# Kernel tuning notes

Hardware: AMD Instinct MI355X
Metric: run time of the kernel (lower is better)

Reference implementation:

```python
import jax, jax.numpy as jnp
import numpy as np

EMBED_DIM = 1024
NUM_HEADS = 16
HEAD_DIM = EMBED_DIM // NUM_HEADS
B, S = 2, 2048


def setup_inputs() -> dict:
    key = jax.random.key(0)
    ks = jax.random.split(key, 9)
    scale = 1.0 / np.sqrt(EMBED_DIM)
    return {
        "x": jax.random.normal(ks[0], (B, S, EMBED_DIM), dtype=jnp.float32),
        "Wq": jax.random.normal(ks[1], (EMBED_DIM, EMBED_DIM), dtype=jnp.float32) * scale,
        "bq": jnp.zeros((EMBED_DIM,), dtype=jnp.float32),
        "Wk": jax.random.normal(ks[2], (EMBED_DIM, EMBED_DIM), dtype=jnp.float32) * scale,
        "bk": jnp.zeros((EMBED_DIM,), dtype=jnp.float32),
        "Wv": jax.random.normal(ks[3], (EMBED_DIM, EMBED_DIM), dtype=jnp.float32) * scale,
        "bv": jnp.zeros((EMBED_DIM,), dtype=jnp.float32),
        "Wo": jax.random.normal(ks[4], (EMBED_DIM, EMBED_DIM), dtype=jnp.float32) * scale,
        "bo": jnp.zeros((EMBED_DIM,), dtype=jnp.float32),
    }


def _split_heads(t):
    # [B, S, E] -> [B, H, S, Dh]
    b, s, _ = t.shape
    return t.reshape(b, s, NUM_HEADS, HEAD_DIM).transpose(0, 2, 1, 3)


def reference(x, Wq, bq, Wk, bk, Wv, bv, Wo, bo):
    q = _split_heads(x @ Wq + bq)
    k = _split_heads(x @ Wk + bk)
    v = _split_heads(x @ Wv + bv)
    scale = jnp.sqrt(jnp.asarray(HEAD_DIM, dtype=x.dtype))
    scores = jnp.einsum("bhqd,bhkd->bhqk", q, k) / scale
    attn = jax.nn.softmax(scores, axis=-1)
    out = jnp.einsum("bhqk,bhkd->bhqd", attn, v)  # [B,H,S,Dh]
    out = out.transpose(0, 2, 1, 3).reshape(x.shape[0], x.shape[1], EMBED_DIM)
    return out @ Wo + bo
```

## Files before the change

### kernel.cpp

```cpp
#include <hip/hip_runtime.h>
#include <math.h>
#include <stdint.h>

typedef __bf16 bf16;
typedef __bf16 bf16x2 __attribute__((ext_vector_type(2)));
typedef __bf16 bf16x4 __attribute__((ext_vector_type(4)));
typedef __bf16 bf16x8 __attribute__((ext_vector_type(8)));
typedef float f32x4 __attribute__((ext_vector_type(4)));
typedef float f32x16 __attribute__((ext_vector_type(16)));

constexpr int E = 1024;
constexpr int S = 2048;
constexpr int H = 16;


__device__ __forceinline__ void gload16(const void* g, void* l) {
  __builtin_amdgcn_global_load_lds(
      (__attribute__((address_space(1))) void*)(uintptr_t)g,
      (__attribute__((address_space(3))) void*)(uint32_t)(uintptr_t)l, 16, 0, 0);
}

__device__ __forceinline__ f32x4 mfma16(bf16x8 a, bf16x8 b, f32x4 c) {
  return __builtin_amdgcn_mfma_f32_16x16x32_bf16(a, b, c, 0, 0, 0);
}
__device__ __forceinline__ f32x16 mfma32(bf16x8 a, bf16x8 b, f32x16 c) {
  return __builtin_amdgcn_mfma_f32_32x32x16_bf16(a, b, c, 0, 0, 0);
}

__device__ __forceinline__ float fexp2(float x) {
#if __has_builtin(__builtin_amdgcn_exp2f)
  return __builtin_amdgcn_exp2f(x);
#else
  float r;
  asm("v_exp_f32 %0, %1" : "=v"(r) : "v"(x));
  return r;
#endif
}

__device__ __forceinline__ uint32_t pkbf(float lo, float hi) {
  bf16x2 p;
  p[0] = (bf16)lo;
  p[1] = (bf16)hi;
  return __builtin_bit_cast(uint32_t, p);
}

__global__ __launch_bounds__(256) void cast_x(const float* __restrict__ x,
                                              bf16* __restrict__ o) {
  const size_t i = ((size_t)blockIdx.x * 256 + threadIdx.x) * 8;
  const float4 a = *(const float4*)(x + i);
  const float4 b = *(const float4*)(x + i + 4);
  bf16x8 r;
  r[0] = (bf16)a.x; r[1] = (bf16)a.y; r[2] = (bf16)a.z; r[3] = (bf16)a.w;
  r[4] = (bf16)b.x; r[5] = (bf16)b.y; r[6] = (bf16)b.z; r[7] = (bf16)b.w;
  *(bf16x8*)(o + i) = r;
}

__global__ __launch_bounds__(256) void transpose_cast_w(
    const float* __restrict__ W0, const float* __restrict__ W1,
    const float* __restrict__ W2, const float* __restrict__ W3,
    bf16* __restrict__ T0, bf16* __restrict__ T1, bf16* __restrict__ T2,
    bf16* __restrict__ T3) {
  const float* W;
  bf16* T;
  switch (blockIdx.z) {
    case 0: W = W0; T = T0; break;
    case 1: W = W1; T = T1; break;
    case 2: W = W2; T = T2; break;
    default: W = W3; T = T3; break;
  }
  __shared__ float t[64][65];
  const int k0 = blockIdx.y * 64, n0 = blockIdx.x * 64;
  const int tr = threadIdx.x >> 4;
  const int tc = (threadIdx.x & 15) * 4;
#pragma unroll
  for (int u = 0; u < 4; ++u) {
    const float4 v = *(const float4*)(W + (size_t)(k0 + tr + u * 16) * E + n0 + tc);
    t[tr + u * 16][tc + 0] = v.x;
    t[tr + u * 16][tc + 1] = v.y;
    t[tr + u * 16][tc + 2] = v.z;
    t[tr + u * 16][tc + 3] = v.w;
  }
  __syncthreads();
#pragma unroll
  for (int u = 0; u < 4; ++u) {
    const int n = tr + u * 16;
    bf16x4 o;
#pragma unroll
    for (int i = 0; i < 4; ++i) o[i] = (bf16)t[tc + i][n];
    *(bf16x4*)(T + (size_t)(n0 + n) * E + k0 + tc) = o;
  }
}

__global__ __launch_bounds__(256) void gemm_qkv(const bf16* __restrict__ A,
                                                const bf16* __restrict__ Wt,
                                                const float* __restrict__ bq,
                                                const float* __restrict__ bk,
                                                const float* __restrict__ bv,
                                                bf16* __restrict__ qo,
                                                bf16* __restrict__ ko,
                                                bf16* __restrict__ vo) {
  __shared__ __attribute__((aligned(16))) bf16 Asm[128 * 32];
  __shared__ __attribute__((aligned(16))) bf16 Bsm[128 * 32];
  const int z = blockIdx.z;
  const bf16* Bt = Wt + (size_t)z * E * E;
  const float* bias = (z == 0) ? bq : (z == 1) ? bk : bv;
  const int tid = threadIdx.x;
  const int w = tid >> 6, lane = tid & 63, quad = lane >> 4, ln = lane & 15;
  const int bm = blockIdx.y * 128, bn = blockIdx.x * 128;
  const int wr = w >> 1, wc = w & 1;
  const int srow = w * 32 + (lane >> 2);
  const int scol = (lane & 3) * 8;
  const bf16* Ag = A + (size_t)(bm + srow) * E + scol;
  const bf16* Bg = Bt + (size_t)(bn + srow) * E + scol;
  f32x4 acc[4][4] = {};

  for (int k0 = 0; k0 < E; k0 += 32) {
    gload16(Ag + k0, &Asm[(w * 32) * 32]);
    gload16(Ag + k0 + (size_t)16 * E, &Asm[(w * 32 + 16) * 32]);
    gload16(Bg + k0, &Bsm[(w * 32) * 32]);
    gload16(Bg + k0 + (size_t)16 * E, &Bsm[(w * 32 + 16) * 32]);
    __syncthreads();
    bf16x8 af[4], bfr[4];
#pragma unroll
    for (int t = 0; t < 4; ++t) {
      af[t] = *(const bf16x8*)&Asm[(wr * 64 + t * 16 + ln) * 32 + quad * 8];
      bfr[t] = *(const bf16x8*)&Bsm[(wc * 64 + t * 16 + ln) * 32 + quad * 8];
    }
#pragma unroll
    for (int rt = 0; rt < 4; ++rt)
#pragma unroll
      for (int ct = 0; ct < 4; ++ct)
        acc[rt][ct] = mfma16(af[rt], bfr[ct], acc[rt][ct]);
    __syncthreads();
  }

  const float scl = (z == 0) ? 0.18033688f : 1.0f;
  const int hglob = (bn + wc * 64) >> 6;
  float bvv[4];
#pragma unroll
  for (int ct = 0; ct < 4; ++ct) bvv[ct] = bias[bn + wc * 64 + ct * 16 + ln];

#pragma unroll
  for (int rt = 0; rt < 4; ++rt) {
    const int row0 = bm + wr * 64 + rt * 16 + quad * 4;
    const int bb = row0 >> 11;
    const int rl = row0 & 2047;
    const size_t hb = (size_t)(bb * 16 + hglob) * 131072;
#pragma unroll
    for (int ct = 0; ct < 4; ++ct) {
      if (z == 2) {
        const int mt = ct >> 1, ln32 = ((ct & 1) << 4) | ln;
        const int tau = rl >> 6, hfv = (rl >> 3) & 1, j0 = rl & 7;
        bf16x4 p;
#pragma unroll
        for (int r = 0; r < 4; ++r) p[r] = (bf16)(acc[rt][ct][r] + bvv[ct]);
        *(bf16x4*)&vo[hb + (size_t)((tau * 8 + mt * 4 + rt) * 512 +
                                    hfv * 256 + ln32 * 8 + j0)] = p;
      } else {
        bf16* o = (z == 0) ? qo : ko;
        const int t = rl >> 5, ln0 = rl & 31;
        const size_t base =
            hb + (size_t)((t * 4 + ct) * 512 + (ln >> 3) * 256 + (ln & 7));
#pragma unroll
        for (int r = 0; r < 4; ++r)
          o[base + (ln0 + r) * 8] = (bf16)((acc[rt][ct][r] + bvv[ct]) * scl);
      }
    }
  }
}

__global__ __launch_bounds__(256) void gemm_wo(const bf16* __restrict__ A,
                                               const bf16* __restrict__ Bt,
                                               const float* __restrict__ bias,
                                               float* __restrict__ C) {
  __shared__ __attribute__((aligned(16))) bf16 Asm[64 * 32];
  __shared__ __attribute__((aligned(16))) bf16 Bsm[128 * 32];
  const int tid = threadIdx.x;
  const int w = tid >> 6, lane = tid & 63, quad = lane >> 4, ln = lane & 15;
  const int bm = blockIdx.y * 64, bn = blockIdx.x * 128;
  const int wr = w >> 1, wc = w & 1;
  const int sr = lane >> 2, sc = (lane & 3) * 8;
  const bf16* Ag = A + (size_t)(bm + w * 16 + sr) * E + sc;
  const bf16* Bg = Bt + (size_t)(bn + w * 32 + sr) * E + sc;
  f32x4 acc[2][4] = {};

  for (int k0 = 0; k0 < E; k0 += 32) {
    gload16(Ag + k0, &Asm[(w * 16) * 32]);
    gload16(Bg + k0, &Bsm[(w * 32) * 32]);
    gload16(Bg + k0 + (size_t)16 * E, &Bsm[(w * 32 + 16) * 32]);
    __syncthreads();
    bf16x8 af[2], bfr[4];
#pragma unroll
    for (int t = 0; t < 2; ++t)
      af[t] = *(const bf16x8*)&Asm[(wr * 32 + t * 16 + ln) * 32 + quad * 8];
#pragma unroll
    for (int t = 0; t < 4; ++t)
      bfr[t] = *(const bf16x8*)&Bsm[(wc * 64 + t * 16 + ln) * 32 + quad * 8];
#pragma unroll
    for (int rt = 0; rt < 2; ++rt)
#pragma unroll
      for (int ct = 0; ct < 4; ++ct)
        acc[rt][ct] = mfma16(af[rt], bfr[ct], acc[rt][ct]);
    __syncthreads();
  }

  float bvv[4];
#pragma unroll
  for (int ct = 0; ct < 4; ++ct) bvv[ct] = bias[bn + wc * 64 + ct * 16 + ln];
#pragma unroll
  for (int rt = 0; rt < 2; ++rt) {
    const int row0 = bm + wr * 32 + rt * 16 + quad * 4;
#pragma unroll
    for (int ct = 0; ct < 4; ++ct) {
      const int c = bn + wc * 64 + ct * 16 + ln;
#pragma unroll
      for (int r = 0; r < 4; ++r)
        C[(size_t)(row0 + r) * E + c] = acc[rt][ct][r] + bvv[ct];
    }
  }
}

__global__ __launch_bounds__(512, 4) void attn_mfma(const bf16* __restrict__ Qf,
                                                    const bf16* __restrict__ Kf,
                                                    const bf16* __restrict__ Vf,
                                                    bf16* __restrict__ Og) {
  __shared__ __attribute__((aligned(16))) char smem[33792];

  const int tid = threadIdx.x;
  const int w = tid >> 6, lane = tid & 63, ln = lane & 31, hf = lane >> 5;
  const int qi = w & 3, ki = w >> 2;
  const int tq = blockIdx.x * 4 + qi;
  const int h = blockIdx.y, b = blockIdx.z;
  const size_t fb = (size_t)(b * H + h) * 131072;

  bf16x8 qf[4];
  {
    const bf16* qb = Qf + fb + (size_t)tq * 2048 + lane * 8;
#pragma unroll
    for (int c = 0; c < 4; ++c) qf[c] = *(const bf16x8*)(qb + c * 512);
  }

  const bf16* Ksrc = Kf + fb + qi * 1024 + lane * 8;
  const int dstoff = ki * 4096 + qi * 1024;
  const bf16* Vg = Vf + fb + (size_t)ki * 16 * 4096 + lane * 8;

  float lpart = 0.f;
  f32x16 oacc[2] = {};

#define STAGE(i, buf)                                                  \
  do {                                                                 \
    const size_t toff = (size_t)(ki * 16 + (i)) * 4096;                \
    bf16* kd = (bf16*)(smem + (buf) * 16384) + dstoff;                 \
    gload16(Ksrc + toff, kd);                                          \
    gload16(Ksrc + toff + 512, kd + 512);                              \
  } while (0)

  STAGE(0, 0);
  __syncthreads();

#pragma unroll 2
  for (int i = 0; i < 16; ++i) {
    const int cur = i & 1;
    const bf16* vt8 = Vg + (size_t)i * 4096;

    bf16x8 vfr[2][2];
#pragma unroll
    for (int vt = 0; vt < 2; ++vt)
#pragma unroll
      for (int cl = 0; cl < 2; ++cl)
        vfr[vt][cl] = *(const bf16x8*)(vt8 + (vt * 4 + 0 * 2 + cl) * 512);

    if (i < 15) STAGE(i + 1, cur ^ 1);
    const bf16* Ks = (const bf16*)(smem + cur * 16384) + ki * 4096;

#pragma unroll
    for (int mt = 0; mt < 2; ++mt) {
      if (mt == 1) {
#pragma unroll
        for (int vt = 0; vt < 2; ++vt)
#pragma unroll
          for (int cl = 0; cl < 2; ++cl)
            vfr[vt][cl] = *(const bf16x8*)(vt8 + (vt * 4 + 2 + cl) * 512);
      }

      f32x16 st = {};
      __builtin_amdgcn_s_setprio(1);
#pragma unroll
      for (int c = 0; c < 4; ++c)
        st = mfma32(*(const bf16x8*)&Ks[(mt * 4 + c) * 512 + lane * 8], qf[c],
                    st);
      __builtin_amdgcn_s_setprio(0);

      float pe[16];
#pragma unroll
      for (int r = 0; r < 16; ++r) pe[r] = fexp2(st[r]);
      lpart += (((pe[0] + pe[1]) + (pe[2] + pe[3])) +
                ((pe[4] + pe[5]) + (pe[6] + pe[7]))) +
               (((pe[8] + pe[9]) + (pe[10] + pe[11])) +
                ((pe[12] + pe[13]) + (pe[14] + pe[15])));

      bf16x8 pb[2];
#pragma unroll
      for (int cl = 0; cl < 2; ++cl) {
        uint32_t a01 = pkbf(pe[cl * 8 + 0], pe[cl * 8 + 1]);
        uint32_t a23 = pkbf(pe[cl * 8 + 2], pe[cl * 8 + 3]);
        uint32_t b01 = pkbf(pe[cl * 8 + 4], pe[cl * 8 + 5]);
        uint32_t b23 = pkbf(pe[cl * 8 + 6], pe[cl * 8 + 7]);
        auto r0 = __builtin_amdgcn_permlane32_swap(a01, b01, false, false);
        auto r1 = __builtin_amdgcn_permlane32_swap(a23, b23, false, false);
        union {
          bf16x8 v;
          uint32_t u[4];
        } pu;
        pu.u[0] = r0[0];
        pu.u[1] = r1[0];
        pu.u[2] = r0[1];
        pu.u[3] = r1[1];
        pb[cl] = pu.v;
      }

      __builtin_amdgcn_s_setprio(1);
#pragma unroll
      for (int vt = 0; vt < 2; ++vt) {
        oacc[vt] = mfma32(vfr[vt][0], pb[0], oacc[vt]);
        oacc[vt] = mfma32(vfr[vt][1], pb[1], oacc[vt]);
      }
      __builtin_amdgcn_s_setprio(0);
    }
    __syncthreads();
  }
#undef STAGE

  float* Ocmb = (float*)smem;
  float* Lcmb = (float*)(smem + 32768);
  if (ki == 1) {
#pragma unroll
    for (int vt = 0; vt < 2; ++vt)
#pragma unroll
      for (int r = 0; r < 16; ++r)
        Ocmb[qi * 2048 + (vt * 16 + r) * 64 + lane] = oacc[vt][r];
    Lcmb[qi * 64 + lane] = lpart;
  }
  __syncthreads();
  if (ki == 0) {
#pragma unroll
    for (int vt = 0; vt < 2; ++vt)
#pragma unroll
      for (int r = 0; r < 16; ++r)
        oacc[vt][r] += Ocmb[qi * 2048 + (vt * 16 + r) * 64 + lane];
    lpart += Lcmb[qi * 64 + lane];

    lpart += __shfl_xor(lpart, 32);
    const float inv = 1.0f / lpart;

    bf16* orow = Og + ((size_t)b * S + (size_t)tq * 32 + ln) * E + h * 64;
#pragma unroll
    for (int vt = 0; vt < 2; ++vt) {
#pragma unroll
      for (int g = 0; g < 4; ++g) {
        bf16x4 o;
#pragma unroll
        for (int j = 0; j < 4; ++j) o[j] = (bf16)(oacc[vt][g * 4 + j] * inv);
        *(bf16x4*)&orow[vt * 32 + g * 8 + hf * 4] = o;
      }
    }
  }
}

extern "C" void kernel_launch(void* const* d_in, const int* in_sizes, int n_in,
                              void* d_out, int out_size, void* d_ws, size_t ws_size,
                              hipStream_t stream) {
  const float* x = (const float*)d_in[0];
  const float* Wq = (const float*)d_in[1];
  const float* bq = (const float*)d_in[2];
  const float* Wk = (const float*)d_in[3];
  const float* bk = (const float*)d_in[4];
  const float* Wv = (const float*)d_in[5];
  const float* bv = (const float*)d_in[6];
  const float* Wo = (const float*)d_in[7];
  const float* bo = (const float*)d_in[8];

  const size_t ME = (size_t)4096 * 1024;
  const size_t WE = (size_t)1024 * 1024;
  bf16* xb = (bf16*)d_ws;
  bf16* wqt = xb + ME;
  bf16* wkt = wqt + WE;
  bf16* wvt = wkt + WE;
  bf16* wot = wvt + WE;
  bf16* qb = wot + WE;
  bf16* kb = qb + ME;
  bf16* vt = kb + ME;
  bf16* ab = vt + ME;

  cast_x<<<2048, 256, 0, stream>>>(x, xb);
  transpose_cast_w<<<dim3(16, 16, 4), 256, 0, stream>>>(Wq, Wk, Wv, Wo, wqt, wkt,
                                                        wvt, wot);
  gemm_qkv<<<dim3(8, 32, 3), 256, 0, stream>>>(xb, wqt, bq, bk, bv, qb, kb, vt);
  attn_mfma<<<dim3(S / 128, H, 2), 512, 0, stream>>>(qb, kb, vt, ab);
  gemm_wo<<<dim3(8, 64), 256, 0, stream>>>(ab, wot, bo, (float*)d_out);
}
```

Before: 213.1 us.

## Split attention KV range across four wave groups and stage V through LDS

The attention block grows from 512 to 1024 threads, so four wave groups (instead of two) each process a quarter of the key sequence. Each iteration now handles a single 32-key tile per wave. V tiles are staged into LDS with async global-to-LDS loads alongside K, replacing direct per-wave global loads of V. Partial outputs and softmax denominators are combined through a two-level LDS reduction with extra barriers. This raises parallelism and LDS usage to 66 KB per block, at the cost of more synchronisation and lower occupancy per CU.

Result: slower. 310.0 us (+45.4%).

```diff
diff --git a/kernel.cpp b/kernel.cpp
--- a/kernel.cpp
+++ b/kernel.cpp
@@ -220,11 +220,10 @@
   }
 }
 
-__global__ __launch_bounds__(512, 4) void attn_mfma(const bf16* __restrict__ Qf,
-                                                    const bf16* __restrict__ Kf,
-                                                    const bf16* __restrict__ Vf,
-                                                    bf16* __restrict__ Og) {
-  __shared__ __attribute__((aligned(16))) char smem[33792];
+__global__ __launch_bounds__(1024, 8) void attn_mfma(
+    const bf16* __restrict__ Qf, const bf16* __restrict__ Kf,
+    const bf16* __restrict__ Vf, bf16* __restrict__ Og) {
+  __shared__ __attribute__((aligned(16))) char smem[67584];
 
   const int tid = threadIdx.x;
   const int w = tid >> 6, lane = tid & 63, ln = lane & 31, hf = lane >> 5;
@@ -240,19 +239,22 @@
     for (int c = 0; c < 4; ++c) qf[c] = *(const bf16x8*)(qb + c * 512);
   }
 
-  const bf16* Ksrc = Kf + fb + qi * 1024 + lane * 8;
-  const int dstoff = ki * 4096 + qi * 1024;
-  const bf16* Vg = Vf + fb + (size_t)ki * 16 * 4096 + lane * 8;
+  const bf16* Ksrc = Kf + fb + lane * 8;
+  const bf16* Vsrc = Vf + fb + lane * 8;
+  const int mtv = qi >> 1, half = qi & 1;
 
   float lpart = 0.f;
   f32x16 oacc[2] = {};
 
-#define STAGE(i, buf)                                                  \
-  do {                                                                 \
-    const size_t toff = (size_t)(ki * 16 + (i)) * 4096;                \
-    bf16* kd = (bf16*)(smem + (buf) * 16384) + dstoff;                 \
-    gload16(Ksrc + toff, kd);                                          \
-    gload16(Ksrc + toff + 512, kd + 512);                              \
+#define STAGE(i, buf)                                                        \
+  do {                                                                       \
+    const int t = ki * 16 + (i);                                             \
+    bf16* base = (bf16*)smem + (buf) * 16384;                                \
+    gload16(Ksrc + (size_t)t * 2048 + qi * 512,                              \
+            base + ki * 2048 + qi * 512);                                    \
+    gload16(Vsrc + (size_t)(((t >> 1) * 8 + mtv * 4 + ((i) & 1) * 2) * 512 + \
+                            half * 512),                                     \
+            base + 8192 + ki * 2048 + mtv * 1024 + half * 512);              \
   } while (0)
 
   STAGE(0, 0);
@@ -261,94 +263,99 @@
 #pragma unroll 2
   for (int i = 0; i < 16; ++i) {
     const int cur = i & 1;
-    const bf16* vt8 = Vg + (size_t)i * 4096;
-
-    bf16x8 vfr[2][2];
+    if (i < 15) STAGE(i + 1, cur ^ 1);
+    const bf16* Kc = (const bf16*)smem + cur * 16384 + ki * 2048;
+    const bf16* Vc = Kc + 8192;
+
+    f32x16 st = {};
+    __builtin_amdgcn_s_setprio(1);
+#pragma unroll
+    for (int c = 0; c < 4; ++c)
+      st = mfma32(*(const bf16x8*)&Kc[c * 512 + lane * 8], qf[c], st);
+    __builtin_amdgcn_s_setprio(0);
+
+    float pe[16];
+#pragma unroll
+    for (int r = 0; r < 16; ++r) pe[r] = fexp2(st[r]);
+    lpart += (((pe[0] + pe[1]) + (pe[2] + pe[3])) +
+              ((pe[4] + pe[5]) + (pe[6] + pe[7]))) +
+             (((pe[8] + pe[9]) + (pe[10] + pe[11])) +
+              ((pe[12] + pe[13]) + (pe[14] + pe[15])));
+
+    bf16x8 pb[2];
+#pragma unroll
+    for (int cl = 0; cl < 2; ++cl) {
+      uint32_t a01 = pkbf(pe[cl * 8 + 0], pe[cl * 8 + 1]);
+      uint32_t a23 = pkbf(pe[cl * 8 + 2], pe[cl * 8 + 3]);
+      uint32_t b01 = pkbf(pe[cl * 8 + 4], pe[cl * 8 + 5]);
+      uint32_t b23 = pkbf(pe[cl * 8 + 6], pe[cl * 8 + 7]);
+      auto r0 = __builtin_amdgcn_permlane32_swap(a01, b01, false, false);
+      auto r1 = __builtin_amdgcn_permlane32_swap(a23, b23, false, false);
+      union {
+        bf16x8 v;
+        uint32_t u[4];
+      } pu;
+      pu.u[0] = r0[0];
+      pu.u[1] = r1[0];
+      pu.u[2] = r0[1];
+      pu.u[3] = r1[1];
+      pb[cl] = pu.v;
+    }
+
+    __builtin_amdgcn_s_setprio(1);
+#pragma unroll
+    for (int vt = 0; vt < 2; ++vt) {
+      oacc[vt] = mfma32(*(const bf16x8*)&Vc[vt * 1024 + lane * 8], pb[0],
+                        oacc[vt]);
+      oacc[vt] = mfma32(*(const bf16x8*)&Vc[vt * 1024 + 512 + lane * 8], pb[1],
+                        oacc[vt]);
+    }
+    __builtin_amdgcn_s_setprio(0);
+
+    __syncthreads();
+  }
+#undef STAGE
+
+  float* Oc = (float*)smem;
+  float* Lc = (float*)(smem + 65536);
+  if (ki >= 2) {
+    const int s = qi * 2 + (ki - 2);
 #pragma unroll
     for (int vt = 0; vt < 2; ++vt)
 #pragma unroll
-      for (int cl = 0; cl < 2; ++cl)
-        vfr[vt][cl] = *(const bf16x8*)(vt8 + (vt * 4 + 0 * 2 + cl) * 512);
-
-    if (i < 15) STAGE(i + 1, cur ^ 1);
-    const bf16* Ks = (const bf16*)(smem + cur * 16384) + ki * 4096;
-
-#pragma unroll
-    for (int mt = 0; mt < 2; ++mt) {
-      if (mt == 1) {
-#pragma unroll
-        for (int vt = 0; vt < 2; ++vt)
-#pragma unroll
-          for (int cl = 0; cl < 2; ++cl)
-            vfr[vt][cl] = *(const bf16x8*)(vt8 + (vt * 4 + 2 + cl) * 512);
-      }
-
-      f32x16 st = {};
-      __builtin_amdgcn_s_setprio(1);
-#pragma unroll
-      for (int c = 0; c < 4; ++c)
-        st = mfma32(*(const bf16x8*)&Ks[(mt * 4 + c) * 512 + lane * 8], qf[c],
-                    st);
-      __builtin_amdgcn_s_setprio(0);
-
-      float pe[16];
-#pragma unroll
-      for (int r = 0; r < 16; ++r) pe[r] = fexp2(st[r]);
-      lpart += (((pe[0] + pe[1]) + (pe[2] + pe[3])) +
-                ((pe[4] + pe[5]) + (pe[6] + pe[7]))) +
-               (((pe[8] + pe[9]) + (pe[10] + pe[11])) +
-                ((pe[12] + pe[13]) + (pe[14] + pe[15])));
-
-      bf16x8 pb[2];
-#pragma unroll
-      for (int cl = 0; cl < 2; ++cl) {
-        uint32_t a01 = pkbf(pe[cl * 8 + 0], pe[cl * 8 + 1]);
-        uint32_t a23 = pkbf(pe[cl * 8 + 2], pe[cl * 8 + 3]);
-        uint32_t b01 = pkbf(pe[cl * 8 + 4], pe[cl * 8 + 5]);
-        uint32_t b23 = pkbf(pe[cl * 8 + 6], pe[cl * 8 + 7]);
-        auto r0 = __builtin_amdgcn_permlane32_swap(a01, b01, false, false);
-        auto r1 = __builtin_amdgcn_permlane32_swap(a23, b23, false, false);
-        union {
-          bf16x8 v;
-          uint32_t u[4];
-        } pu;
-        pu.u[0] = r0[0];
-        pu.u[1] = r1[0];
-        pu.u[2] = r0[1];
-        pu.u[3] = r1[1];
-        pb[cl] = pu.v;
-      }
-
-      __builtin_amdgcn_s_setprio(1);
-#pragma unroll
-      for (int vt = 0; vt < 2; ++vt) {
-        oacc[vt] = mfma32(vfr[vt][0], pb[0], oacc[vt]);
-        oacc[vt] = mfma32(vfr[vt][1], pb[1], oacc[vt]);
-      }
-      __builtin_amdgcn_s_setprio(0);
-    }
-    __syncthreads();
-  }
-#undef STAGE
-
-  float* Ocmb = (float*)smem;
-  float* Lcmb = (float*)(smem + 32768);
+      for (int r = 0; r < 16; ++r)
+        Oc[s * 2048 + (vt * 16 + r) * 64 + lane] = oacc[vt][r];
+    Lc[s * 64 + lane] = lpart;
+  }
+  __syncthreads();
+  if (ki < 2) {
+    const int s = qi * 2 + ki;
+#pragma unroll
+    for (int vt = 0; vt < 2; ++vt)
+#pragma unroll
+      for (int r = 0; r < 16; ++r)
+        oacc[vt][r] += Oc[s * 2048 + (vt * 16 + r) * 64 + lane];
+    lpart += Lc[s * 64 + lane];
+  }
+  __syncthreads();
   if (ki == 1) {
+    const int s = qi * 2;
 #pragma unroll
     for (int vt = 0; vt < 2; ++vt)
 #pragma unroll
       for (int r = 0; r < 16; ++r)
-        Ocmb[qi * 2048 + (vt * 16 + r) * 64 + lane] = oacc[vt][r];
-    Lcmb[qi * 64 + lane] = lpart;
+        Oc[s * 2048 + (vt * 16 + r) * 64 + lane] = oacc[vt][r];
+    Lc[s * 64 + lane] = lpart;
   }
   __syncthreads();
   if (ki == 0) {
+    const int s = qi * 2;
 #pragma unroll
     for (int vt = 0; vt < 2; ++vt)
 #pragma unroll
       for (int r = 0; r < 16; ++r)
-        oacc[vt][r] += Ocmb[qi * 2048 + (vt * 16 + r) * 64 + lane];
-    lpart += Lcmb[qi * 64 + lane];
+        oacc[vt][r] += Oc[s * 2048 + (vt * 16 + r) * 64 + lane];
+    lpart += Lc[s * 64 + lane];
 
     lpart += __shfl_xor(lpart, 32);
     const float inv = 1.0f / lpart;
@@ -396,6 +403,6 @@
   transpose_cast_w<<<dim3(16, 16, 4), 256, 0, stream>>>(Wq, Wk, Wv, Wo, wqt, wkt,
                                                         wvt, wot);
   gemm_qkv<<<dim3(8, 32, 3), 256, 0, stream>>>(xb, wqt, bq, bk, bv, qb, kb, vt);
-  attn_mfma<<<dim3(S / 128, H, 2), 512, 0, stream>>>(qb, kb, vt, ab);
+  attn_mfma<<<dim3(S / 128, H, 2), 1024, 0, stream>>>(qb, kb, vt, ab);
   gemm_wo<<<dim3(8, 64), 256, 0, stream>>>(ab, wot, bo, (float*)d_out);
 }
```
